# Performance work log

Measured on AMD Instinct MI355X. Metric: run time of the kernel, lower is better.

## Reference

```python
import jax, jax.numpy as jnp
import numpy as np

N_NODES = 100_000
N_EDGES = 1_600_000  # random edges; self-loops appended (add_self_edges_networkx)
IN_FEATS = 64
N_HIDDEN = 64
N_CLASSES = 40


def setup_inputs() -> dict:
    key = jax.random.key(0)
    ks = jax.random.split(key, 10)
    features = jax.random.normal(ks[0], (N_NODES, IN_FEATS), jnp.float32)
    self_loops = jnp.arange(N_NODES, dtype=jnp.int32)
    src = jnp.concatenate([jax.random.randint(ks[1], (N_EDGES,), 0, N_NODES, jnp.int32), self_loops])
    dst = jnp.concatenate([jax.random.randint(ks[2], (N_EDGES,), 0, N_NODES, jnp.int32), self_loops])
    labels = jax.random.randint(ks[3], (N_NODES,), 0, N_CLASSES, jnp.int32)
    mask = jnp.ones((N_NODES,), bool)
    s = 0.05
    W0 = jax.random.normal(ks[4], (IN_FEATS, N_HIDDEN), jnp.float32) * s
    b0 = jnp.zeros((N_HIDDEN,), jnp.float32)
    W1 = jax.random.normal(ks[5], (N_HIDDEN, N_HIDDEN), jnp.float32) * s
    b1 = jnp.zeros((N_HIDDEN,), jnp.float32)
    W2 = jax.random.normal(ks[6], (N_HIDDEN, N_CLASSES), jnp.float32) * s
    b2 = jnp.zeros((N_CLASSES,), jnp.float32)
    return {"features": features, "W0": W0, "b0": b0, "W1": W1, "b1": b1,
            "W2": W2, "b2": b2, "src": src, "dst": dst,
            "labels": labels, "mask": mask}


def reference(features, W0, b0, W1, b1, W2, b2, src, dst, labels, mask):
    # gcn_msg: pass src 'h'; gcn_reduce: sum over incoming messages;
    # NodeApplyModule: linear (+ activation on non-final layers).
    def gcn_layer(h, W, b, act):
        agg = jax.ops.segment_sum(h[src], dst, num_segments=N_NODES)  # gather -> sum reduce
        h = agg @ W + b
        return jax.nn.relu(h) if act else h

    h = gcn_layer(features, W0, b0, act=True)
    h = gcn_layer(h, W1, b1, act=True)
    rep = gcn_layer(h, W2, b2, act=False)  # [N, n_classes]

    # loss: fn_reduce=log_softmax over dim=0 (as written in the source), nll sum / count
    logp = jax.nn.log_softmax(rep, axis=0)
    picked = jnp.take_along_axis(logp, labels[:, None].astype(jnp.int32), axis=1)[:, 0]
    maskf = mask.astype(jnp.float32)
    loss = -jnp.sum(picked * maskf) / jnp.sum(maskf)
    return rep, loss
```

## Files before the change

kernel.cpp:

```cpp
#include <hip/hip_runtime.h>
#include <hip/hip_bf16.h>
#include <hip/hip_fp16.h>

#define NCLS 40

typedef __attribute__((ext_vector_type(8))) _Float16 half8;
typedef __attribute__((ext_vector_type(2))) _Float16 half2h;
union H2U { half2h h; unsigned u; };

#define EPB 16384
#define MAXB1 128
#define MAXNB 104

__global__ __launch_bounds__(256) void hist_and_gemm(
        const int* __restrict__ dst, int E, int nb, int* __restrict__ blockHist, int nB1,
        const float* __restrict__ X, const float* __restrict__ W,
        _Float16* __restrict__ out, int N) {
    __shared__ int cnt[4][MAXNB];
    int t = threadIdx.x;
    if ((int)blockIdx.x < nB1) {
        for (int i = t; i < 4 * MAXNB; i += 256) cnt[i / MAXNB][i % MAXNB] = 0;
        __syncthreads();
        int bk = t & 3;
        int base = blockIdx.x * EPB;
        int end = min(base + EPB, E);
        for (int i = base + t; i < end; i += 256) atomicAdd(&cnt[bk][dst[i] >> 10], 1);
        __syncthreads();
        for (int i = t; i < nb; i += 256)
            blockHist[blockIdx.x * nb + i] = cnt[0][i] + cnt[1][i] + cnt[2][i] + cnt[3][i];
        return;
    }
    int bid = blockIdx.x - nB1;
    int nBlocks = gridDim.x - nB1;
    int lane = t & 63;
    int waveId = (bid * 256 + t) >> 6;
    int nWaves = (nBlocks * 256) >> 6;
    int p = lane & 31;

    H2U wh[32];
#pragma unroll
    for (int j = 0; j < 32; ++j)
        wh[j].h = half2h{(_Float16)W[(2 * j) * 64 + lane], (_Float16)W[(2 * j + 1) * 64 + lane]};

    const float2* Xf = (const float2*)X;
    auto loadX = [&](int row) -> H2U {
        H2U r; r.u = 0;
        if (row < N) {
            float2 f = Xf[(size_t)row * 32 + p];
            r.h = half2h{(_Float16)f.x, (_Float16)f.y};
        }
        return r;
    };
    int row = waveId;
    H2U xp = loadX(row);
    for (; row < N; row += nWaves) {
        H2U nxt = loadX(row + nWaves);
        float y0 = 0.f, y1 = 0.f;
#pragma unroll
        for (int j2 = 0; j2 < 32; j2 += 2) {
            H2U r0, r1;
            r0.u = __builtin_amdgcn_readlane(xp.u, j2);
            r1.u = __builtin_amdgcn_readlane(xp.u, j2 + 1);
            y0 = __builtin_amdgcn_fdot2(r0.h, wh[j2].h, y0, false);
            y1 = __builtin_amdgcn_fdot2(r1.h, wh[j2 + 1].h, y1, false);
        }
        out[(size_t)row * 64 + lane] = (_Float16)(y0 + y1);
        xp = nxt;
    }
}

__global__ void bucket_scan(const int* __restrict__ blockHist, int nB1, int nb,
                            int* __restrict__ blockBase, int* __restrict__ bucketOffs,
                            int* __restrict__ offs, int N, int E, int* __restrict__ red32) {
    __shared__ int h[MAXB1 * MAXNB];
    __shared__ int btot[MAXNB];
    __shared__ int boffs[MAXNB + 1];
    int t = threadIdx.x;
    if (t < 128) red32[t] = 0;
    int total = nB1 * nb;
    for (int i = t; i < total; i += 128) h[i] = blockHist[i];
    __syncthreads();
    for (int b = t; b < nb; b += 128) {
        int run = 0;
        for (int i = 0; i < nB1; ++i) { int v = h[i * nb + b]; h[i * nb + b] = run; run += v; }
        btot[b] = run;
    }
    __syncthreads();
    if (t == 0) {
        int run = 0;
        for (int b = 0; b < nb; ++b) { boffs[b] = run; run += btot[b]; }
        boffs[nb] = run;
    }
    __syncthreads();
    for (int b = t; b < nb; b += 128) {
        int bo = boffs[b];
        for (int i = 0; i < nB1; ++i) h[i * nb + b] += bo;
    }
    __syncthreads();
    for (int i = t; i < total; i += 128) blockBase[i] = h[i];
    for (int b = t; b <= nb; b += 128) bucketOffs[b] = boffs[b];
    if (t == 0) offs[N] = E;
}

__global__ void bucket_place(const int* __restrict__ src, const int* __restrict__ dst, int E,
                             int nb, const int* __restrict__ blockBase,
                             unsigned* __restrict__ tmp) {
    __shared__ int cur[MAXNB];
    int t = threadIdx.x;
    for (int i = t; i < nb; i += 256) cur[i] = blockBase[blockIdx.x * nb + i];
    __syncthreads();
    int base = blockIdx.x * EPB;
    int end = min(base + EPB, E);
    for (int i = base + t; i < end; i += 256) {
        int d = dst[i];
        int s = src[i];
        unsigned pack = ((unsigned)(d & 1023) << 17) | (unsigned)s;
        int pos = atomicAdd(&cur[d >> 10], 1);
        tmp[pos] = pack;
    }
}

__global__ __launch_bounds__(512) void bucket_finalize(const unsigned* __restrict__ tmp,
                                                       const int* __restrict__ bucketOffs,
                                                       int N, int* __restrict__ offs,
                                                       int* __restrict__ esrc) {
    __shared__ int cnt[1024];
    __shared__ int wsum[8];
    int b = blockIdx.x;
    int t = threadIdx.x;
    int bstart = bucketOffs[b], bend = bucketOffs[b + 1];
    cnt[t] = 0;
    cnt[t + 512] = 0;
    __syncthreads();
    for (int i = bstart + t; i < bend; i += 512) atomicAdd(&cnt[tmp[i] >> 17], 1);
    __syncthreads();
    int c0 = cnt[2 * t], c1 = cnt[2 * t + 1];
    int s = c0 + c1;
    int lane = t & 63, w = t >> 6;
    int ssc = s;
    for (int off = 1; off < 64; off <<= 1) {
        int v = __shfl_up(ssc, off, 64);
        if (lane >= off) ssc += v;
    }
    if (lane == 63) wsum[w] = ssc;
    __syncthreads();
    int wo = 0;
#pragma unroll
    for (int k = 0; k < 8; ++k)
        if (k < w) wo += wsum[k];
    int excl = (ssc - s) + wo + bstart;
    __syncthreads();
    int node0 = (b << 10) + 2 * t;
    if (node0 < N) offs[node0] = excl;
    if (node0 + 1 < N) offs[node0 + 1] = excl + c0;
    cnt[2 * t] = excl;
    cnt[2 * t + 1] = excl + c0;
    __syncthreads();
    for (int i = bstart + t; i < bend; i += 512) {
        unsigned p = tmp[i];
        int pos = atomicAdd(&cnt[p >> 17], 1);
        esrc[pos] = (int)(p & 0x1FFFFu);
    }
}

__global__ __launch_bounds__(256) void gemm_fdot(const void* __restrict__ X, int xHalf,
                                                 const float* __restrict__ W,
                                                 const float* __restrict__ bias,
                                                 void* __restrict__ out, int outHalf,
                                                 int N, int FO) {
    int lane = threadIdx.x & 63;
    int waveId = (blockIdx.x * blockDim.x + threadIdx.x) >> 6;
    int nWaves = (gridDim.x * blockDim.x) >> 6;
    int cl = lane < FO ? lane : 0;
    int p = lane & 31;

    H2U wh[32];
#pragma unroll
    for (int j = 0; j < 32; ++j)
        wh[j].h = half2h{(_Float16)W[(2 * j) * FO + cl], (_Float16)W[(2 * j + 1) * FO + cl]};
    float gb = 0.f;
    if (bias != nullptr && lane < FO) gb = bias[lane];

    const unsigned* Xh = (const unsigned*)X;
    const float2* Xf = (const float2*)X;
    float* outF = (float*)out;
    _Float16* outH = (_Float16*)out;

    auto loadX = [&](int row) -> H2U {
        H2U r; r.u = 0;
        if (row < N) {
            if (xHalf) r.u = Xh[(size_t)row * 32 + p];
            else {
                float2 f = Xf[(size_t)row * 32 + p];
                r.h = half2h{(_Float16)f.x, (_Float16)f.y};
            }
        }
        return r;
    };

    int row = waveId;
    H2U xp = loadX(row);
    for (; row < N; row += nWaves) {
        H2U nxt = loadX(row + nWaves);
        float y0 = gb, y1 = 0.f;
#pragma unroll
        for (int j2 = 0; j2 < 32; j2 += 2) {
            H2U r0, r1;
            r0.u = __builtin_amdgcn_readlane(xp.u, j2);
            r1.u = __builtin_amdgcn_readlane(xp.u, j2 + 1);
            y0 = __builtin_amdgcn_fdot2(r0.h, wh[j2].h, y0, false);
            y1 = __builtin_amdgcn_fdot2(r1.h, wh[j2 + 1].h, y1, false);
        }
        float y = y0 + y1;
        if (lane < FO) {
            if (outHalf) outH[(size_t)row * FO + lane] = (_Float16)y;
            else         outF[(size_t)row * FO + lane] = y;
        }
        xp = nxt;
    }
}

#define ACC_PAIR(word, ae, ao)                                        \
    do {                                                              \
        H2U _p; _p.u = (word);                                        \
        (ae) = __builtin_amdgcn_fdot2(_p.h, selE.h, (ae), false);     \
        (ao) = __builtin_amdgcn_fdot2(_p.h, selO.h, (ao), false);     \
    } while (0)

__global__ void agg64h_kernel(const _Float16* __restrict__ t, const int* __restrict__ offs,
                              const int* __restrict__ esrc, const float* __restrict__ bias,
                              _Float16* __restrict__ out, int N) {
    int gid = blockIdx.x * blockDim.x + threadIdx.x;
    int node = gid >> 6;
    if (node >= N) return;
    int lane = threadIdx.x & 63;
    int sub = lane >> 3;
    int c8 = lane & 7;
    int beg = offs[node], end = offs[node + 1];
    H2U selE, selO;
    selE.h = half2h{(_Float16)1.f, (_Float16)0.f};
    selO.h = half2h{(_Float16)0.f, (_Float16)1.f};
    float a[8];
#pragma unroll
    for (int k = 0; k < 8; ++k) a[k] = 0.f;
    int j = beg + sub;
    for (; j + 8 < end; j += 16) {
        int s0 = esrc[j];
        int s1 = esrc[j + 8];
        uint4 v0 = *(const uint4*)(t + (size_t)s0 * 64 + c8 * 8);
        uint4 v1 = *(const uint4*)(t + (size_t)s1 * 64 + c8 * 8);
        ACC_PAIR(v0.x, a[0], a[1]); ACC_PAIR(v0.y, a[2], a[3]);
        ACC_PAIR(v0.z, a[4], a[5]); ACC_PAIR(v0.w, a[6], a[7]);
        ACC_PAIR(v1.x, a[0], a[1]); ACC_PAIR(v1.y, a[2], a[3]);
        ACC_PAIR(v1.z, a[4], a[5]); ACC_PAIR(v1.w, a[6], a[7]);
    }
    if (j < end) {
        int s0 = esrc[j];
        uint4 v0 = *(const uint4*)(t + (size_t)s0 * 64 + c8 * 8);
        ACC_PAIR(v0.x, a[0], a[1]); ACC_PAIR(v0.y, a[2], a[3]);
        ACC_PAIR(v0.z, a[4], a[5]); ACC_PAIR(v0.w, a[6], a[7]);
    }
#pragma unroll
    for (int k = 0; k < 8; ++k) {
        a[k] += __shfl_down(a[k], 32, 64);
        a[k] += __shfl_down(a[k], 16, 64);
        a[k] += __shfl_down(a[k], 8, 64);
    }
    if (sub == 0) {
        half8 hv;
#pragma unroll
        for (int k = 0; k < 8; ++k) {
            float v = fmaxf(a[k] + bias[c8 * 8 + k], 0.f);
            hv[k] = (_Float16)v;
        }
        *(half8*)(out + (size_t)node * 64 + c8 * 8) = hv;
    }
}

__global__ void agg40h_kernel(const _Float16* __restrict__ u, const int* __restrict__ offs,
                              const int* __restrict__ esrc, const float* __restrict__ bias,
                              float* __restrict__ rep, int N) {
    int gid = blockIdx.x * blockDim.x + threadIdx.x;
    int node = gid >> 6;
    if (node >= N) return;
    int lane = threadIdx.x & 63;
    int sub = lane >> 3;
    int c8 = lane & 7;
    int beg = offs[node], end = offs[node + 1];
    H2U selE, selO;
    selE.h = half2h{(_Float16)1.f, (_Float16)0.f};
    selO.h = half2h{(_Float16)0.f, (_Float16)1.f};
    float a[8];
#pragma unroll
    for (int k = 0; k < 8; ++k) a[k] = 0.f;
    if (c8 < 5) {
        int j = beg + sub;
        for (; j + 8 < end; j += 16) {
            int s0 = esrc[j];
            int s1 = esrc[j + 8];
            uint4 v0 = *(const uint4*)(u + (size_t)s0 * 40 + c8 * 8);
            uint4 v1 = *(const uint4*)(u + (size_t)s1 * 40 + c8 * 8);
            ACC_PAIR(v0.x, a[0], a[1]); ACC_PAIR(v0.y, a[2], a[3]);
            ACC_PAIR(v0.z, a[4], a[5]); ACC_PAIR(v0.w, a[6], a[7]);
            ACC_PAIR(v1.x, a[0], a[1]); ACC_PAIR(v1.y, a[2], a[3]);
            ACC_PAIR(v1.z, a[4], a[5]); ACC_PAIR(v1.w, a[6], a[7]);
        }
        if (j < end) {
            int s0 = esrc[j];
            uint4 v0 = *(const uint4*)(u + (size_t)s0 * 40 + c8 * 8);
            ACC_PAIR(v0.x, a[0], a[1]); ACC_PAIR(v0.y, a[2], a[3]);
            ACC_PAIR(v0.z, a[4], a[5]); ACC_PAIR(v0.w, a[6], a[7]);
        }
    }
#pragma unroll
    for (int k = 0; k < 8; ++k) {
        a[k] += __shfl_down(a[k], 32, 64);
        a[k] += __shfl_down(a[k], 16, 64);
        a[k] += __shfl_down(a[k], 8, 64);
    }
    if (sub == 0 && c8 < 5) {
        float* po = rep + (size_t)node * NCLS + c8 * 8;
        float4 r0, r1;
        r0.x = a[0] + bias[c8 * 8 + 0]; r0.y = a[1] + bias[c8 * 8 + 1];
        r0.z = a[2] + bias[c8 * 8 + 2]; r0.w = a[3] + bias[c8 * 8 + 3];
        r1.x = a[4] + bias[c8 * 8 + 4]; r1.y = a[5] + bias[c8 * 8 + 5];
        r1.z = a[6] + bias[c8 * 8 + 6]; r1.w = a[7] + bias[c8 * 8 + 7];
        *(float4*)(po) = r0;
        *(float4*)(po + 4) = r1;
    }
}

__global__ void loss_pass(const float* __restrict__ rep, const int* __restrict__ labels, int N,
                          double* __restrict__ colSum, double* __restrict__ pickedSum,
                          int* __restrict__ cnt) {
    const int G = 8;
    const int ROWS = 512;
    int t = threadIdx.x;
    int c = t % NCLS;
    int g = t / NCLS;
    int base = blockIdx.x * ROWS;
    int lim = min(base + ROWS, N);
    double sumLoc = 0.0, pickLoc = 0.0;
    int cntLoc = 0;
    for (int r = base + g; r < lim; r += G) {
        float v = rep[(size_t)r * NCLS + c];
        sumLoc += exp((double)v);
        if (labels[r] == c) { pickLoc += (double)v; cntLoc++; }
    }
    __shared__ double colP[G][NCLS];
    __shared__ int cntP[G][NCLS];
    __shared__ double waveP[5];
    colP[g][c] = sumLoc;
    cntP[g][c] = cntLoc;
    __syncthreads();
    if (g == 0) {
        double tot = 0.0;
        int ctot = 0;
        for (int gg = 0; gg < G; ++gg) { tot += colP[gg][c]; ctot += cntP[gg][c]; }
        atomicAdd(&colSum[c], tot);
        if (ctot) atomicAdd(&cnt[c], ctot);
    }
    double wv = pickLoc;
    for (int off = 32; off; off >>= 1) wv += __shfl_down(wv, off, 64);
    if ((t & 63) == 0) waveP[t >> 6] = wv;
    __syncthreads();
    if (t == 0) {
        double s = 0.0;
        for (int i = 0; i < 5; ++i) s += waveP[i];
        atomicAdd(pickedSum, s);
    }
}

__global__ void finalize_kernel(const double* __restrict__ colSum, const int* __restrict__ cnt,
                                const double* __restrict__ pickedSum, int N,
                                float* __restrict__ lossOut) {
    int t = threadIdx.x;
    double term = 0.0;
    if (t < NCLS) term = (double)cnt[t] * log(colSum[t]);
    for (int off = 32; off; off >>= 1) term += __shfl_down(term, off, 64);
    if (t == 0) lossOut[0] = (float)((term - pickedSum[0]) / (double)N);
}

extern "C" void kernel_launch(void* const* d_in, const int* in_sizes, int n_in,
                              void* d_out, int out_size, void* d_ws, size_t ws_size,
                              hipStream_t stream) {
    const float* features = (const float*)d_in[0];
    const float* W0 = (const float*)d_in[1];
    const float* b0 = (const float*)d_in[2];
    const float* W1 = (const float*)d_in[3];
    const float* b1 = (const float*)d_in[4];
    const float* W2 = (const float*)d_in[5];
    const float* b2 = (const float*)d_in[6];
    const int* src = (const int*)d_in[7];
    const int* dst = (const int*)d_in[8];
    const int* labels = (const int*)d_in[9];

    const int N = in_sizes[0] / 64;
    const int E = in_sizes[7];
    const int NC = in_sizes[6];

    char* ws = (char*)d_ws;
    size_t off = 0;
    auto alloc = [&](size_t bytes) -> void* {
        void* p = ws + off;
        off = (off + bytes + 255) & ~(size_t)255;
        return p;
    };
    int* offs      = (int*)alloc((size_t)(N + 1) * 4);
    int* esrc      = (int*)alloc((size_t)E * 4);
    _Float16* bufA = (_Float16*)alloc((size_t)N * 64 * 2);
    _Float16* bufB = (_Float16*)alloc((size_t)N * 64 * 2);
    unsigned* tmp  = (unsigned*)alloc((size_t)E * 4);
    int* blockHist = (int*)alloc((size_t)MAXB1 * MAXNB * 4);
    int* blockBase = (int*)alloc((size_t)MAXB1 * MAXNB * 4);
    int* bucketOffs= (int*)alloc((size_t)(MAXNB + 1) * 4);
    char* red      = (char*)alloc(512);
    double* colSum    = (double*)red;
    double* pickedSum = (double*)(red + 320);
    int* cntRed       = (int*)(red + 328);

    float* rep = (float*)d_out;
    float* lossOut = rep + (size_t)N * NC;

    const int nb  = (N + 1023) >> 10;
    const int nB1 = (E + EPB - 1) / EPB;

    hist_and_gemm<<<nB1 + 2048, 256, 0, stream>>>(dst, E, nb, blockHist, nB1,
                                                  features, W0, bufA, N);
    bucket_scan<<<1, 128, 0, stream>>>(blockHist, nB1, nb, blockBase, bucketOffs, offs, N, E,
                                       (int*)red);
    bucket_place<<<nB1, 256, 0, stream>>>(src, dst, E, nb, blockBase, tmp);
    bucket_finalize<<<nb, 512, 0, stream>>>(tmp, bucketOffs, N, offs, esrc);

    const int nodeWaveBlocks = (N * 64 + 255) / 256;

    agg64h_kernel<<<nodeWaveBlocks, 256, 0, stream>>>(bufA, offs, esrc, b0, bufB, N);
    gemm_fdot<<<2048, 256, 0, stream>>>(bufB, 1, W1, nullptr, bufA, 1, N, 64);
    agg64h_kernel<<<nodeWaveBlocks, 256, 0, stream>>>(bufA, offs, esrc, b1, bufB, N);
    gemm_fdot<<<2048, 256, 0, stream>>>(bufB, 1, W2, nullptr, bufA, 1, N, NC);
    agg40h_kernel<<<nodeWaveBlocks, 256, 0, stream>>>(bufA, offs, esrc, b2, rep, N);

    loss_pass<<<(N + 511) / 512, 320, 0, stream>>>(rep, labels, N, colSum, pickedSum, cntRed);
    finalize_kernel<<<1, 64, 0, stream>>>(colSum, cntRed, pickedSum, N, lossOut);
}
```

Measured before the change: 373.8 us.

## Aggregate edges per 64-node group with LDS atomics and reorder final layer

Replaces the wave-per-node gather kernels with a block-per-64-node-group kernel. The group's edge range is split evenly across 32 slots of 8 threads, and partial sums are flushed into shared-memory accumulators with atomics whenever the destination changes. The destination-local index is packed into esrc to support this, and a prefetch pipeline reads two edges ahead, which needs padding at the end of esrc. The last layer now aggregates 64-wide features before the W2 GEMM rather than after, with the bias added in gemm_fdot. This balances work across skewed degrees and removes the cross-lane shuffle reductions, at the cost of LDS atomic contention and a wider final aggregation.

```diff
diff --git a/kernel.cpp b/kernel.cpp
--- a/kernel.cpp
+++ b/kernel.cpp
@@ -71,7 +71,8 @@
 
 __global__ void bucket_scan(const int* __restrict__ blockHist, int nB1, int nb,
                             int* __restrict__ blockBase, int* __restrict__ bucketOffs,
-                            int* __restrict__ offs, int N, int E, int* __restrict__ red32) {
+                            int* __restrict__ offs, int N, int E, int* __restrict__ red32,
+                            int* __restrict__ esrc) {
     __shared__ int h[MAXB1 * MAXNB];
     __shared__ int btot[MAXNB];
     __shared__ int boffs[MAXNB + 1];
@@ -99,7 +100,8 @@
     __syncthreads();
     for (int i = t; i < total; i += 128) blockBase[i] = h[i];
     for (int b = t; b <= nb; b += 128) bucketOffs[b] = boffs[b];
-    if (t == 0) offs[N] = E;
+    if (t == 0) { offs[N] = E; }
+    if (t < 8) esrc[E + t] = 0;
 }
 
 __global__ void bucket_place(const int* __restrict__ src, const int* __restrict__ dst, int E,
@@ -159,7 +161,7 @@
     for (int i = bstart + t; i < bend; i += 512) {
         unsigned p = tmp[i];
         int pos = atomicAdd(&cnt[p >> 17], 1);
-        esrc[pos] = (int)(p & 0x1FFFFu);
+        esrc[pos] = (int)((((p >> 17) & 127u) << 17) | (p & 0x1FFFFu));
     }
 }
 
@@ -227,106 +229,79 @@
         (ao) = __builtin_amdgcn_fdot2(_p.h, selO.h, (ao), false);     \
     } while (0)
 
-__global__ void agg64h_kernel(const _Float16* __restrict__ t, const int* __restrict__ offs,
-                              const int* __restrict__ esrc, const float* __restrict__ bias,
-                              _Float16* __restrict__ out, int N) {
-    int gid = blockIdx.x * blockDim.x + threadIdx.x;
-    int node = gid >> 6;
-    if (node >= N) return;
-    int lane = threadIdx.x & 63;
-    int sub = lane >> 3;
-    int c8 = lane & 7;
-    int beg = offs[node], end = offs[node + 1];
+#define GNODES 64
+#define GSH 6
+#define AST 66
+
+template <int MODE>
+__global__ __launch_bounds__(256) void agg_lds_kernel(
+        const _Float16* __restrict__ t, const int* __restrict__ offs,
+        const int* __restrict__ esrc, const float* __restrict__ bias,
+        _Float16* __restrict__ out, int N) {
+    __shared__ float acc[GNODES * AST];
+    int tid = threadIdx.x;
+    int g0 = blockIdx.x << GSH;
+    int g1 = min(g0 + GNODES, N);
+    for (int i = tid; i < GNODES * AST; i += 256) acc[i] = 0.f;
+    int beg = offs[g0];
+    int end = offs[g1];
+    __syncthreads();
+
+    int nE = end - beg;
+    int chunk = (nE + 31) >> 5;
+    int slot = tid >> 3;
+    int oct = tid & 7;
+    int e0 = beg + slot * chunk;
+    int e1 = min(e0 + chunk, end);
+
     H2U selE, selO;
     selE.h = half2h{(_Float16)1.f, (_Float16)0.f};
     selO.h = half2h{(_Float16)0.f, (_Float16)1.f};
+
     float a[8];
 #pragma unroll
     for (int k = 0; k < 8; ++k) a[k] = 0.f;
-    int j = beg + sub;
-    for (; j + 8 < end; j += 16) {
-        int s0 = esrc[j];
-        int s1 = esrc[j + 8];
-        uint4 v0 = *(const uint4*)(t + (size_t)s0 * 64 + c8 * 8);
-        uint4 v1 = *(const uint4*)(t + (size_t)s1 * 64 + c8 * 8);
-        ACC_PAIR(v0.x, a[0], a[1]); ACC_PAIR(v0.y, a[2], a[3]);
-        ACC_PAIR(v0.z, a[4], a[5]); ACC_PAIR(v0.w, a[6], a[7]);
-        ACC_PAIR(v1.x, a[0], a[1]); ACC_PAIR(v1.y, a[2], a[3]);
-        ACC_PAIR(v1.z, a[4], a[5]); ACC_PAIR(v1.w, a[6], a[7]);
-    }
-    if (j < end) {
-        int s0 = esrc[j];
-        uint4 v0 = *(const uint4*)(t + (size_t)s0 * 64 + c8 * 8);
-        ACC_PAIR(v0.x, a[0], a[1]); ACC_PAIR(v0.y, a[2], a[3]);
-        ACC_PAIR(v0.z, a[4], a[5]); ACC_PAIR(v0.w, a[6], a[7]);
-    }
-#pragma unroll
-    for (int k = 0; k < 8; ++k) {
-        a[k] += __shfl_down(a[k], 32, 64);
-        a[k] += __shfl_down(a[k], 16, 64);
-        a[k] += __shfl_down(a[k], 8, 64);
-    }
-    if (sub == 0) {
-        half8 hv;
-#pragma unroll
-        for (int k = 0; k < 8; ++k) {
-            float v = fmaxf(a[k] + bias[c8 * 8 + k], 0.f);
-            hv[k] = (_Float16)v;
-        }
-        *(half8*)(out + (size_t)node * 64 + c8 * 8) = hv;
-    }
-}
-
-__global__ void agg40h_kernel(const _Float16* __restrict__ u, const int* __restrict__ offs,
-                              const int* __restrict__ esrc, const float* __restrict__ bias,
-                              float* __restrict__ rep, int N) {
-    int gid = blockIdx.x * blockDim.x + threadIdx.x;
-    int node = gid >> 6;
-    if (node >= N) return;
-    int lane = threadIdx.x & 63;
-    int sub = lane >> 3;
-    int c8 = lane & 7;
-    int beg = offs[node], end = offs[node + 1];
-    H2U selE, selO;
-    selE.h = half2h{(_Float16)1.f, (_Float16)0.f};
-    selO.h = half2h{(_Float16)0.f, (_Float16)1.f};
-    float a[8];
-#pragma unroll
-    for (int k = 0; k < 8; ++k) a[k] = 0.f;
-    if (c8 < 5) {
-        int j = beg + sub;
-        for (; j + 8 < end; j += 16) {
-            int s0 = esrc[j];
-            int s1 = esrc[j + 8];
-            uint4 v0 = *(const uint4*)(u + (size_t)s0 * 40 + c8 * 8);
-            uint4 v1 = *(const uint4*)(u + (size_t)s1 * 40 + c8 * 8);
-            ACC_PAIR(v0.x, a[0], a[1]); ACC_PAIR(v0.y, a[2], a[3]);
-            ACC_PAIR(v0.z, a[4], a[5]); ACC_PAIR(v0.w, a[6], a[7]);
-            ACC_PAIR(v1.x, a[0], a[1]); ACC_PAIR(v1.y, a[2], a[3]);
-            ACC_PAIR(v1.z, a[4], a[5]); ACC_PAIR(v1.w, a[6], a[7]);
-        }
-        if (j < end) {
-            int s0 = esrc[j];
-            uint4 v0 = *(const uint4*)(u + (size_t)s0 * 40 + c8 * 8);
-            ACC_PAIR(v0.x, a[0], a[1]); ACC_PAIR(v0.y, a[2], a[3]);
-            ACC_PAIR(v0.z, a[4], a[5]); ACC_PAIR(v0.w, a[6], a[7]);
-        }
-    }
-#pragma unroll
-    for (int k = 0; k < 8; ++k) {
-        a[k] += __shfl_down(a[k], 32, 64);
-        a[k] += __shfl_down(a[k], 16, 64);
-        a[k] += __shfl_down(a[k], 8, 64);
-    }
-    if (sub == 0 && c8 < 5) {
-        float* po = rep + (size_t)node * NCLS + c8 * 8;
-        float4 r0, r1;
-        r0.x = a[0] + bias[c8 * 8 + 0]; r0.y = a[1] + bias[c8 * 8 + 1];
-        r0.z = a[2] + bias[c8 * 8 + 2]; r0.w = a[3] + bias[c8 * 8 + 3];
-        r1.x = a[4] + bias[c8 * 8 + 4]; r1.y = a[5] + bias[c8 * 8 + 5];
-        r1.z = a[6] + bias[c8 * 8 + 6]; r1.w = a[7] + bias[c8 * 8 + 7];
-        *(float4*)(po) = r0;
-        *(float4*)(po + 4) = r1;
+
+    if (e0 < e1) {
+        int cur = -1;
+        int pA = esrc[e0];
+        int pB = esrc[e0 + 1];
+        uint4 vA = *(const uint4*)(t + (size_t)(pA & 0x1FFFF) * 64 + oct * 8);
+        for (int e = e0; e < e1; ++e) {
+            int pC = esrc[e + 2];
+            uint4 vB = *(const uint4*)(t + (size_t)(pB & 0x1FFFF) * 64 + oct * 8);
+            int dl = (pA >> 17) & (GNODES - 1);
+            if (dl != cur) {
+                if (cur >= 0) {
+                    float* fp = &acc[cur * AST + oct * 8];
+#pragma unroll
+                    for (int k = 0; k < 8; ++k) { atomicAdd(&fp[k], a[k]); a[k] = 0.f; }
+                }
+                cur = dl;
+            }
+            ACC_PAIR(vA.x, a[0], a[1]); ACC_PAIR(vA.y, a[2], a[3]);
+            ACC_PAIR(vA.z, a[4], a[5]); ACC_PAIR(vA.w, a[6], a[7]);
+            pA = pB; pB = pC; vA = vB;
+        }
+        float* fp = &acc[cur * AST + oct * 8];
+#pragma unroll
+        for (int k = 0; k < 8; ++k) atomicAdd(&fp[k], a[k]);
+    }
+    __syncthreads();
+
+    for (int u = tid; u < GNODES * 8; u += 256) {
+        int node = u >> 3, oc = u & 7;
+        int gn = g0 + node;
+        if (gn < N) {
+            half8 hv;
+#pragma unroll
+            for (int k = 0; k < 8; ++k) {
+                float v = acc[node * AST + oc * 8 + k];
+                if (MODE == 0) v = fmaxf(v + bias[oc * 8 + k], 0.f);
+                hv[k] = (_Float16)v;
+            }
+            *(half8*)(out + (size_t)gn * 64 + oc * 8) = hv;
+        }
     }
 }
 
@@ -407,7 +382,7 @@
         return p;
     };
     int* offs      = (int*)alloc((size_t)(N + 1) * 4);
-    int* esrc      = (int*)alloc((size_t)E * 4);
+    int* esrc      = (int*)alloc((size_t)(E + 8) * 4);
     _Float16* bufA = (_Float16*)alloc((size_t)N * 64 * 2);
     _Float16* bufB = (_Float16*)alloc((size_t)N * 64 * 2);
     unsigned* tmp  = (unsigned*)alloc((size_t)E * 4);
@@ -428,17 +403,17 @@
     hist_and_gemm<<<nB1 + 2048, 256, 0, stream>>>(dst, E, nb, blockHist, nB1,
                                                   features, W0, bufA, N);
     bucket_scan<<<1, 128, 0, stream>>>(blockHist, nB1, nb, blockBase, bucketOffs, offs, N, E,
-                                       (int*)red);
+                                       (int*)red, esrc);
     bucket_place<<<nB1, 256, 0, stream>>>(src, dst, E, nb, blockBase, tmp);
     bucket_finalize<<<nb, 512, 0, stream>>>(tmp, bucketOffs, N, offs, esrc);
 
-    const int nodeWaveBlocks = (N * 64 + 255) / 256;
-
-    agg64h_kernel<<<nodeWaveBlocks, 256, 0, stream>>>(bufA, offs, esrc, b0, bufB, N);
+    const int nGroups = (N + GNODES - 1) >> GSH;
+
+    agg_lds_kernel<0><<<nGroups, 256, 0, stream>>>(bufA, offs, esrc, b0, bufB, N);
     gemm_fdot<<<2048, 256, 0, stream>>>(bufB, 1, W1, nullptr, bufA, 1, N, 64);
-    agg64h_kernel<<<nodeWaveBlocks, 256, 0, stream>>>(bufA, offs, esrc, b1, bufB, N);
-    gemm_fdot<<<2048, 256, 0, stream>>>(bufB, 1, W2, nullptr, bufA, 1, N, NC);
-    agg40h_kernel<<<nodeWaveBlocks, 256, 0, stream>>>(bufA, offs, esrc, b2, rep, N);
+    agg_lds_kernel<0><<<nGroups, 256, 0, stream>>>(bufA, offs, esrc, b1, bufB, N);
+    agg_lds_kernel<1><<<nGroups, 256, 0, stream>>>(bufB, offs, esrc, nullptr, bufA, N);
+    gemm_fdot<<<2048, 256, 0, stream>>>(bufA, 1, W2, b2, rep, 0, N, NC);
 
     loss_pass<<<(N + 511) / 512, 320, 0, stream>>>(rep, labels, N, colSum, pickedSum, cntRed);
     finalize_kernel<<<1, 64, 0, stream>>>(colSum, cntRed, pickedSum, N, lossOut);
```

Result: slower. 449.9 us (+20.4%).
